# Performance work log

Measured on AMD Instinct MI355X. Metric: run time of the kernel, lower is better.

Reference implementation:

```python
import jax, jax.numpy as jnp
import numpy as np

TEMPERATURE = 0.5


def setup_inputs() -> dict:
    key = jax.random.key(0)
    k1, k2 = jax.random.split(key)
    emb = jax.random.normal(k1, (16384, 128), dtype=jnp.float32)
    emb = emb / jnp.linalg.norm(emb, axis=1, keepdims=True)  # L2-normalized, per docstring
    labels = jax.random.randint(k2, (16384,), 0, 64, dtype=jnp.int64)
    return {"embeddings": emb, "partition_labels": labels}


def reference(embeddings, partition_labels):
    n = embeddings.shape[0]
    # [N, N] similarity matrix, scaled by temperature
    sim = jnp.matmul(embeddings, embeddings.T) / TEMPERATURE
    exp_sim = jnp.exp(sim)
    eye = jnp.eye(n, dtype=bool)
    pos_mask = (partition_labels[None, :] == partition_labels[:, None]) & ~eye
    # numerator: sum of exp over positives; denominator: sum over all k != i
    pos_sum = jnp.sum(jnp.where(pos_mask, exp_sim, 0.0), axis=1)
    all_sum = jnp.sum(jnp.where(~eye, exp_sim, 0.0), axis=1)
    valid = jnp.any(pos_mask, axis=1)
    loss_i = -(jnp.log(pos_sum) - jnp.log(all_sum))
    n_valid = jnp.sum(valid)
    total = jnp.sum(jnp.where(valid, loss_i, 0.0))
    return jnp.where(n_valid > 0, total / n_valid, 0.0)
```

## Files before the change

### kernel.cpp

```cpp
#include <hip/hip_runtime.h>

#define N_EMB 16384
#define DIM 128
#define BM 128
#define BN 128
#define NSPLIT 8
#define CPS (N_EMB / NSPLIT)
#define NCT (CPS / BN)

typedef __bf16 bf16x8 __attribute__((ext_vector_type(8)));
typedef float f32x4 __attribute__((ext_vector_type(4)));
typedef unsigned short us8 __attribute__((ext_vector_type(8)));
typedef unsigned int u32;

#define SCALE 2.8853900817779268f

__device__ inline float fast_exp2(float x) {
#if __has_builtin(__builtin_amdgcn_exp2f)
  return __builtin_amdgcn_exp2f(x);
#else
  return exp2f(x);
#endif
}
__device__ inline float fast_log2(float x) {
#if __has_builtin(__builtin_amdgcn_logf)
  return __builtin_amdgcn_logf(x);
#else
  return log2f(x);
#endif
}

__device__ inline unsigned short f2bf(float f) {
  unsigned int u = __float_as_uint(f);
  u += 0x7fffu + ((u >> 16) & 1u);
  return (unsigned short)(u >> 16);
}

__device__ inline void gll16(const unsigned short* g, unsigned short* l) {
  __builtin_amdgcn_global_load_lds(
      (const __attribute__((address_space(1))) u32*)g,
      (__attribute__((address_space(3))) u32*)l, 16, 0, 0);
}

__device__ inline void stage_tile_fl(const float* __restrict__ src,
                                     unsigned short* __restrict__ dst,
                                     int tid) {
#pragma unroll
  for (int i = 0; i < 8; ++i) {
    int G = i * 256 + tid;
    int col16 = G & 15;
    int quad = (G >> 4) & 3;
    int ks = (G >> 6) & 3;
    int tc = G >> 8;
    const float* p = src + (tc * 16 + col16) * DIM + ks * 32 + quad * 8;
    float4 a = *reinterpret_cast<const float4*>(p);
    float4 b = *reinterpret_cast<const float4*>(p + 4);
    us8 g;
    g[0] = f2bf(a.x); g[1] = f2bf(a.y); g[2] = f2bf(a.z); g[3] = f2bf(a.w);
    g[4] = f2bf(b.x); g[5] = f2bf(b.y); g[6] = f2bf(b.z); g[7] = f2bf(b.w);
    *reinterpret_cast<us8*>(dst + G * 8) = g;
  }
}

__global__ __launch_bounds__(256) void preconv(
    const float* __restrict__ emb, unsigned short* __restrict__ eraw,
    unsigned short* __restrict__ escal) {
  __shared__ unsigned short lds[128 * DIM];
  const int tid = threadIdx.x;
  const size_t base = (size_t)blockIdx.x * (128 * DIM);
  stage_tile_fl(emb + base, lds, tid);
  __syncthreads();
#pragma unroll
  for (int i = 0; i < 8; ++i) {
    int G = i * 256 + tid;
    us8 v = *reinterpret_cast<const us8*>(lds + G * 8);
    *reinterpret_cast<us8*>(eraw + base + G * 8) = v;
    us8 s;
#pragma unroll
    for (int j = 0; j < 8; ++j) {
      float f = __uint_as_float((u32)v[j] << 16) * SCALE;
      s[j] = f2bf(f);
    }
    *reinterpret_cast<us8*>(escal + base + G * 8) = s;
  }
}

__global__ __launch_bounds__(256, 4) void cl_main(
    const unsigned short* __restrict__ eraw,
    const unsigned short* __restrict__ escal,
    const int* __restrict__ labels, float* __restrict__ ws_all,
    float* __restrict__ ws_pos) {
  __shared__ unsigned short lds[BN * DIM];

  const int tid = threadIdx.x;
  const int lane = tid & 63;
  const int w = tid >> 6;
  const int col16 = lane & 15;
  const int quad = lane >> 4;
  const int r0 = blockIdx.x * BM;
  const int cs = blockIdx.y;

  {
    const unsigned short* g = escal + (size_t)r0 * DIM;
#pragma unroll
    for (int i = 0; i < 8; ++i) {
      int chunk = i * 4 + w;
      gll16(g + chunk * 512 + lane * 8, lds + chunk * 512);
    }
  }
  __syncthreads();

  bf16x8 afrag[2][4];
#pragma unroll
  for (int tr = 0; tr < 2; ++tr)
#pragma unroll
    for (int ks = 0; ks < 4; ++ks)
      afrag[tr][ks] = *reinterpret_cast<const bf16x8*>(
          lds + ((w * 2 + tr) * 4 + ks) * 512 + lane * 8);

  int labi[8];
  float all_p[8], pos_p[8];
#pragma unroll
  for (int t = 0; t < 8; ++t) {
    labi[t] = labels[r0 + w * 32 + (t >> 2) * 16 + quad * 4 + (t & 3)];
    all_p[t] = 0.f;
    pos_p[t] = 0.f;
  }

  for (int ct = 0; ct < NCT; ++ct) {
    const int c0 = cs * CPS + ct * BN;
    __syncthreads();
    {
      const unsigned short* g = eraw + (size_t)c0 * DIM;
#pragma unroll
      for (int i = 0; i < 8; ++i) {
        int chunk = i * 4 + w;
        gll16(g + chunk * 512 + lane * 8, lds + chunk * 512);
      }
    }
    __syncthreads();

#pragma unroll
    for (int tc = 0; tc < 8; ++tc) {
      bf16x8 bf[4];
#pragma unroll
      for (int ks = 0; ks < 4; ++ks)
        bf[ks] = *reinterpret_cast<const bf16x8*>(lds + (tc * 4 + ks) * 512 +
                                                  lane * 8);
      int labj = labels[c0 + tc * 16 + col16];
#pragma unroll
      for (int tr = 0; tr < 2; ++tr) {
        f32x4 acc = {0.f, 0.f, 0.f, 0.f};
#pragma unroll
        for (int ks = 0; ks < 4; ++ks)
          acc = __builtin_amdgcn_mfma_f32_16x16x32_bf16(afrag[tr][ks], bf[ks],
                                                        acc, 0, 0, 0);
        const bool diag = (c0 + tc * 16) == (r0 + w * 32 + tr * 16);
#pragma unroll
        for (int r = 0; r < 4; ++r) {
          float e = fast_exp2(acc[r]);
          if (diag && (quad * 4 + r) == col16) e = 0.f;
          all_p[tr * 4 + r] += e;
          pos_p[tr * 4 + r] += (labi[tr * 4 + r] == labj) ? e : 0.f;
        }
      }
    }
  }

#pragma unroll
  for (int t = 0; t < 8; ++t) {
    float a = all_p[t], p = pos_p[t];
#pragma unroll
    for (int m = 8; m >= 1; m >>= 1) {
      a += __shfl_xor(a, m, 64);
      p += __shfl_xor(p, m, 64);
    }
    if (col16 == 0) {
      int row_g = r0 + w * 32 + (t >> 2) * 16 + quad * 4 + (t & 3);
      ws_all[cs * N_EMB + row_g] = a;
      ws_pos[cs * N_EMB + row_g] = p;
    }
  }
}

__global__ __launch_bounds__(1024) void finalize_kernel(
    const float* __restrict__ ws_all, const float* __restrict__ ws_pos,
    float* __restrict__ out) {
  __shared__ float s_t[1024];
  __shared__ int s_c[1024];
  const int tid = threadIdx.x;
  float tot = 0.f;
  int cnt = 0;
  for (int row = tid; row < N_EMB; row += 1024) {
    float a = 0.f, p = 0.f;
#pragma unroll
    for (int s = 0; s < NSPLIT; ++s) {
      a += ws_all[s * N_EMB + row];
      p += ws_pos[s * N_EMB + row];
    }
    if (p > 0.f) {
      tot += fast_log2(a) - fast_log2(p);
      cnt++;
    }
  }
  s_t[tid] = tot;
  s_c[tid] = cnt;
  __syncthreads();
  for (int s = 512; s > 0; s >>= 1) {
    if (tid < s) {
      s_t[tid] += s_t[tid + s];
      s_c[tid] += s_c[tid + s];
    }
    __syncthreads();
  }
  if (tid == 0)
    out[0] =
        (s_c[0] > 0) ? (s_t[0] * 0.6931471805599453f / (float)s_c[0]) : 0.f;
}

extern "C" void kernel_launch(void* const* d_in, const int* in_sizes, int n_in,
                              void* d_out, int out_size, void* d_ws,
                              size_t ws_size, hipStream_t stream) {
  const float* emb = (const float*)d_in[0];
  const int* labels = (const int*)d_in[1];

  unsigned short* eraw = (unsigned short*)d_ws;
  unsigned short* escal = eraw + (size_t)N_EMB * DIM;
  float* ws_all = (float*)(escal + (size_t)N_EMB * DIM);
  float* ws_pos = ws_all + NSPLIT * N_EMB;

  preconv<<<N_EMB / 128, 256, 0, stream>>>(emb, eraw, escal);
  cl_main<<<dim3(N_EMB / BM, NSPLIT), 256, 0, stream>>>(eraw, escal, labels,
                                                        ws_all, ws_pos);
  finalize_kernel<<<1, 1024, 0, stream>>>(ws_all, ws_pos, (float*)d_out);
}
```

Measured before the change: 164.2 us.

## Sort rows by label and compute positive sums only within label groups

Rows are bucketed by label into a permutation, so the dense pass computes only the all-pair exp sums with no label compares or diagonal masking. A separate kernel computes positive sums over the block-diagonal label groups and records the diagonal term, which is subtracted afterwards. The dense kernel also uses 128-thread blocks with each wave holding 64 rows, and the final reduction is split across many blocks. This adds a serial single-block histogram/permutation kernel, extra launches, and a small redundant MFMA pass over the group tiles.

```diff
diff --git a/kernel.cpp b/kernel.cpp
--- a/kernel.cpp
+++ b/kernel.cpp
@@ -2,11 +2,11 @@
 
 #define N_EMB 16384
 #define DIM 128
-#define BM 128
-#define BN 128
 #define NSPLIT 8
 #define CPS (N_EMB / NSPLIT)
+#define BN 128
 #define NCT (CPS / BN)
+#define NLAB 64
 
 typedef __bf16 bf16x8 __attribute__((ext_vector_type(8)));
 typedef float f32x4 __attribute__((ext_vector_type(4)));
@@ -14,6 +14,7 @@
 typedef unsigned int u32;
 
 #define SCALE 2.8853900817779268f
+#define LN2 0.6931471805599453f
 
 __device__ inline float fast_exp2(float x) {
 #if __has_builtin(__builtin_amdgcn_exp2f)
@@ -42,90 +43,89 @@
       (__attribute__((address_space(3))) u32*)l, 16, 0, 0);
 }
 
-__device__ inline void stage_tile_fl(const float* __restrict__ src,
-                                     unsigned short* __restrict__ dst,
-                                     int tid) {
-#pragma unroll
-  for (int i = 0; i < 8; ++i) {
-    int G = i * 256 + tid;
+__global__ __launch_bounds__(1024) void perm_kernel(
+    const int* __restrict__ labels, int* __restrict__ perm,
+    int* __restrict__ gstart) {
+  __shared__ int hist[NLAB];
+  __shared__ int cur[NLAB];
+  const int tid = threadIdx.x;
+  if (tid < NLAB) hist[tid] = 0;
+  __syncthreads();
+  for (int i = tid; i < N_EMB; i += 1024) atomicAdd(&hist[labels[i]], 1);
+  __syncthreads();
+  if (tid == 0) {
+    int s = 0;
+    for (int l = 0; l < NLAB; ++l) {
+      gstart[l] = s;
+      cur[l] = s;
+      s += hist[l];
+    }
+    gstart[NLAB] = s;
+  }
+  __syncthreads();
+  for (int i = tid; i < N_EMB; i += 1024) {
+    int p = atomicAdd(&cur[labels[i]], 1);
+    perm[p] = i;
+  }
+}
+
+__global__ __launch_bounds__(256) void preconv(
+    const float* __restrict__ emb, const int* __restrict__ perm,
+    unsigned short* __restrict__ eraw, unsigned short* __restrict__ escal) {
+  const int tid = threadIdx.x;
+  const int tile = blockIdx.x >> 2;
+  const int part = blockIdx.x & 3;
+  const size_t base = (size_t)tile * (128 * DIM);
+#pragma unroll
+  for (int i = 0; i < 2; ++i) {
+    int G = part * 512 + i * 256 + tid;
     int col16 = G & 15;
-    int quad = (G >> 4) & 3;
+    int qd = (G >> 4) & 3;
     int ks = (G >> 6) & 3;
     int tc = G >> 8;
-    const float* p = src + (tc * 16 + col16) * DIM + ks * 32 + quad * 8;
+    int srow = perm[tile * 128 + tc * 16 + col16];
+    const float* p = emb + (size_t)srow * DIM + ks * 32 + qd * 8;
     float4 a = *reinterpret_cast<const float4*>(p);
     float4 b = *reinterpret_cast<const float4*>(p + 4);
-    us8 g;
+    us8 g, s;
     g[0] = f2bf(a.x); g[1] = f2bf(a.y); g[2] = f2bf(a.z); g[3] = f2bf(a.w);
     g[4] = f2bf(b.x); g[5] = f2bf(b.y); g[6] = f2bf(b.z); g[7] = f2bf(b.w);
-    *reinterpret_cast<us8*>(dst + G * 8) = g;
-  }
-}
-
-__global__ __launch_bounds__(256) void preconv(
-    const float* __restrict__ emb, unsigned short* __restrict__ eraw,
-    unsigned short* __restrict__ escal) {
-  __shared__ unsigned short lds[128 * DIM];
-  const int tid = threadIdx.x;
-  const size_t base = (size_t)blockIdx.x * (128 * DIM);
-  stage_tile_fl(emb + base, lds, tid);
-  __syncthreads();
-#pragma unroll
-  for (int i = 0; i < 8; ++i) {
-    int G = i * 256 + tid;
-    us8 v = *reinterpret_cast<const us8*>(lds + G * 8);
-    *reinterpret_cast<us8*>(eraw + base + G * 8) = v;
-    us8 s;
 #pragma unroll
     for (int j = 0; j < 8; ++j) {
-      float f = __uint_as_float((u32)v[j] << 16) * SCALE;
+      float f = __uint_as_float((u32)g[j] << 16) * SCALE;
       s[j] = f2bf(f);
     }
-    *reinterpret_cast<us8*>(escal + base + G * 8) = s;
-  }
-}
-
-__global__ __launch_bounds__(256, 4) void cl_main(
+    *reinterpret_cast<us8*>(eraw + base + (size_t)G * 8) = g;
+    *reinterpret_cast<us8*>(escal + base + (size_t)G * 8) = s;
+  }
+}
+
+__global__ __launch_bounds__(128, 2) void cl_all(
     const unsigned short* __restrict__ eraw,
-    const unsigned short* __restrict__ escal,
-    const int* __restrict__ labels, float* __restrict__ ws_all,
-    float* __restrict__ ws_pos) {
+    const unsigned short* __restrict__ escal, float* __restrict__ ws_all) {
   __shared__ unsigned short lds[BN * DIM];
-
   const int tid = threadIdx.x;
   const int lane = tid & 63;
   const int w = tid >> 6;
   const int col16 = lane & 15;
   const int quad = lane >> 4;
-  const int r0 = blockIdx.x * BM;
+  const int r0 = blockIdx.x * 128;
   const int cs = blockIdx.y;
 
-  {
-    const unsigned short* g = escal + (size_t)r0 * DIM;
-#pragma unroll
-    for (int i = 0; i < 8; ++i) {
-      int chunk = i * 4 + w;
-      gll16(g + chunk * 512 + lane * 8, lds + chunk * 512);
-    }
-  }
-  __syncthreads();
-
-  bf16x8 afrag[2][4];
-#pragma unroll
-  for (int tr = 0; tr < 2; ++tr)
+  bf16x8 afrag[4][4];
+#pragma unroll
+  for (int tr = 0; tr < 4; ++tr) {
+    const int T = (r0 >> 4) + w * 4 + tr;
+    const unsigned short* p = escal + (size_t)(T >> 3) * (128 * DIM) +
+                              ((T & 7) * 4) * 512 + lane * 8;
 #pragma unroll
     for (int ks = 0; ks < 4; ++ks)
-      afrag[tr][ks] = *reinterpret_cast<const bf16x8*>(
-          lds + ((w * 2 + tr) * 4 + ks) * 512 + lane * 8);
-
-  int labi[8];
-  float all_p[8], pos_p[8];
-#pragma unroll
-  for (int t = 0; t < 8; ++t) {
-    labi[t] = labels[r0 + w * 32 + (t >> 2) * 16 + quad * 4 + (t & 3)];
-    all_p[t] = 0.f;
-    pos_p[t] = 0.f;
-  }
+      afrag[tr][ks] = *reinterpret_cast<const bf16x8*>(p + ks * 512);
+  }
+
+  float all_p[16];
+#pragma unroll
+  for (int t = 0; t < 16; ++t) all_p[t] = 0.f;
 
   for (int ct = 0; ct < NCT; ++ct) {
     const int c0 = cs * CPS + ct * BN;
@@ -133,8 +133,8 @@
     {
       const unsigned short* g = eraw + (size_t)c0 * DIM;
 #pragma unroll
-      for (int i = 0; i < 8; ++i) {
-        int chunk = i * 4 + w;
+      for (int i = 0; i < 16; ++i) {
+        int chunk = i * 2 + w;
         gll16(g + chunk * 512 + lane * 8, lds + chunk * 512);
       }
     }
@@ -142,80 +142,146 @@
 
 #pragma unroll
     for (int tc = 0; tc < 8; ++tc) {
-      bf16x8 bf[4];
+      bf16x8 bfr[4];
 #pragma unroll
       for (int ks = 0; ks < 4; ++ks)
-        bf[ks] = *reinterpret_cast<const bf16x8*>(lds + (tc * 4 + ks) * 512 +
-                                                  lane * 8);
-      int labj = labels[c0 + tc * 16 + col16];
-#pragma unroll
-      for (int tr = 0; tr < 2; ++tr) {
+        bfr[ks] = *reinterpret_cast<const bf16x8*>(lds + (tc * 4 + ks) * 512 +
+                                                   lane * 8);
+#pragma unroll
+      for (int tr = 0; tr < 4; ++tr) {
         f32x4 acc = {0.f, 0.f, 0.f, 0.f};
 #pragma unroll
         for (int ks = 0; ks < 4; ++ks)
-          acc = __builtin_amdgcn_mfma_f32_16x16x32_bf16(afrag[tr][ks], bf[ks],
+          acc = __builtin_amdgcn_mfma_f32_16x16x32_bf16(afrag[tr][ks], bfr[ks],
                                                         acc, 0, 0, 0);
-        const bool diag = (c0 + tc * 16) == (r0 + w * 32 + tr * 16);
-#pragma unroll
-        for (int r = 0; r < 4; ++r) {
-          float e = fast_exp2(acc[r]);
-          if (diag && (quad * 4 + r) == col16) e = 0.f;
-          all_p[tr * 4 + r] += e;
-          pos_p[tr * 4 + r] += (labi[tr * 4 + r] == labj) ? e : 0.f;
+#pragma unroll
+        for (int r = 0; r < 4; ++r)
+          all_p[tr * 4 + r] += fast_exp2(acc[r]);
+      }
+    }
+  }
+
+#pragma unroll
+  for (int t = 0; t < 16; ++t) {
+    float a = all_p[t];
+#pragma unroll
+    for (int m = 8; m >= 1; m >>= 1) a += __shfl_xor(a, m, 64);
+    if (col16 == 0) {
+      int row_g = r0 + w * 64 + (t >> 2) * 16 + quad * 4 + (t & 3);
+      ws_all[cs * N_EMB + row_g] = a;
+    }
+  }
+}
+
+__global__ __launch_bounds__(256) void cl_pos(
+    const unsigned short* __restrict__ eraw,
+    const unsigned short* __restrict__ escal, const int* __restrict__ gstart,
+    float* __restrict__ ws_pos, float* __restrict__ ws_diag) {
+  const int l = blockIdx.x;
+  const int chunk = blockIdx.y;
+  const int gs = gstart[l], ge = gstart[l + 1];
+  const int tid = threadIdx.x;
+  const int lane = tid & 63;
+  const int w = tid >> 6;
+  const int col16 = lane & 15;
+  const int quad = lane >> 4;
+  const int t0 = gs >> 4;
+  const int t1 = (ge + 15) >> 4;
+
+  for (int ta = t0 + chunk * 4 + w; ta < t1; ta += 16) {
+    bf16x8 af[4];
+    const unsigned short* pa = escal + (size_t)(ta >> 3) * (128 * DIM) +
+                               ((ta & 7) * 4) * 512 + lane * 8;
+#pragma unroll
+    for (int ks = 0; ks < 4; ++ks)
+      af[ks] = *reinterpret_cast<const bf16x8*>(pa + ks * 512);
+    const int grow = ta * 16 + quad * 4;
+    float posr[4] = {0.f, 0.f, 0.f, 0.f};
+
+    for (int tb = t0; tb < t1; ++tb) {
+      bf16x8 bfr[4];
+      const unsigned short* pb = eraw + (size_t)(tb >> 3) * (128 * DIM) +
+                                 ((tb & 7) * 4) * 512 + lane * 8;
+#pragma unroll
+      for (int ks = 0; ks < 4; ++ks)
+        bfr[ks] = *reinterpret_cast<const bf16x8*>(pb + ks * 512);
+      f32x4 acc = {0.f, 0.f, 0.f, 0.f};
+#pragma unroll
+      for (int ks = 0; ks < 4; ++ks)
+        acc = __builtin_amdgcn_mfma_f32_16x16x32_bf16(af[ks], bfr[ks], acc, 0,
+                                                      0, 0);
+      const int gcol = tb * 16 + col16;
+      const bool colin = (gcol >= gs) && (gcol < ge);
+#pragma unroll
+      for (int r = 0; r < 4; ++r) {
+        float e = fast_exp2(acc[r]);
+        const int gr = grow + r;
+        if (gcol == gr) {
+          if (colin) ws_diag[gr] = e;
+        } else if (colin) {
+          posr[r] += e;
         }
       }
     }
-  }
-
-#pragma unroll
-  for (int t = 0; t < 8; ++t) {
-    float a = all_p[t], p = pos_p[t];
-#pragma unroll
-    for (int m = 8; m >= 1; m >>= 1) {
-      a += __shfl_xor(a, m, 64);
-      p += __shfl_xor(p, m, 64);
-    }
-    if (col16 == 0) {
-      int row_g = r0 + w * 32 + (t >> 2) * 16 + quad * 4 + (t & 3);
-      ws_all[cs * N_EMB + row_g] = a;
-      ws_pos[cs * N_EMB + row_g] = p;
-    }
-  }
-}
-
-__global__ __launch_bounds__(1024) void finalize_kernel(
+
+#pragma unroll
+    for (int r = 0; r < 4; ++r) {
+      float p = posr[r];
+#pragma unroll
+      for (int m = 8; m >= 1; m >>= 1) p += __shfl_xor(p, m, 64);
+      const int gr = grow + r;
+      if (col16 == 0 && gr >= gs && gr < ge) ws_pos[gr] = p;
+    }
+  }
+}
+
+__global__ __launch_bounds__(256) void fin1(
     const float* __restrict__ ws_all, const float* __restrict__ ws_pos,
-    float* __restrict__ out) {
-  __shared__ float s_t[1024];
-  __shared__ int s_c[1024];
-  const int tid = threadIdx.x;
-  float tot = 0.f;
-  int cnt = 0;
-  for (int row = tid; row < N_EMB; row += 1024) {
-    float a = 0.f, p = 0.f;
-#pragma unroll
-    for (int s = 0; s < NSPLIT; ++s) {
-      a += ws_all[s * N_EMB + row];
-      p += ws_pos[s * N_EMB + row];
-    }
-    if (p > 0.f) {
-      tot += fast_log2(a) - fast_log2(p);
-      cnt++;
-    }
-  }
-  s_t[tid] = tot;
-  s_c[tid] = cnt;
+    const float* __restrict__ ws_diag, float* __restrict__ part_tot,
+    int* __restrict__ part_cnt) {
+  __shared__ float s_t[256];
+  __shared__ int s_c[256];
+  const int tid = threadIdx.x;
+  const int row = blockIdx.x * 256 + tid;
+  float a = 0.f;
+#pragma unroll
+  for (int s = 0; s < NSPLIT; ++s) a += ws_all[s * N_EMB + row];
+  a -= ws_diag[row];
+  const float p = ws_pos[row];
+  float t = 0.f;
+  int c = 0;
+  if (p > 0.f) {
+    t = fast_log2(a) - fast_log2(p);
+    c = 1;
+  }
+  s_t[tid] = t;
+  s_c[tid] = c;
   __syncthreads();
-  for (int s = 512; s > 0; s >>= 1) {
+  for (int s = 128; s > 0; s >>= 1) {
     if (tid < s) {
       s_t[tid] += s_t[tid + s];
       s_c[tid] += s_c[tid + s];
     }
     __syncthreads();
   }
-  if (tid == 0)
-    out[0] =
-        (s_c[0] > 0) ? (s_t[0] * 0.6931471805599453f / (float)s_c[0]) : 0.f;
+  if (tid == 0) {
+    part_tot[blockIdx.x] = s_t[0];
+    part_cnt[blockIdx.x] = s_c[0];
+  }
+}
+
+__global__ __launch_bounds__(64) void fin2(const float* __restrict__ part_tot,
+                                           const int* __restrict__ part_cnt,
+                                           float* __restrict__ out) {
+  const int tid = threadIdx.x;
+  float t = part_tot[tid];
+  int c = part_cnt[tid];
+#pragma unroll
+  for (int m = 32; m >= 1; m >>= 1) {
+    t += __shfl_xor(t, m, 64);
+    c += __shfl_xor(c, m, 64);
+  }
+  if (tid == 0) out[0] = (c > 0) ? (t * LN2 / (float)c) : 0.f;
 }
 
 extern "C" void kernel_launch(void* const* d_in, const int* in_sizes, int n_in,
@@ -228,9 +294,18 @@
   unsigned short* escal = eraw + (size_t)N_EMB * DIM;
   float* ws_all = (float*)(escal + (size_t)N_EMB * DIM);
   float* ws_pos = ws_all + NSPLIT * N_EMB;
-
-  preconv<<<N_EMB / 128, 256, 0, stream>>>(emb, eraw, escal);
-  cl_main<<<dim3(N_EMB / BM, NSPLIT), 256, 0, stream>>>(eraw, escal, labels,
-                                                        ws_all, ws_pos);
-  finalize_kernel<<<1, 1024, 0, stream>>>(ws_all, ws_pos, (float*)d_out);
-}
+  float* ws_diag = ws_pos + N_EMB;
+  float* part_tot = ws_diag + N_EMB;
+  int* part_cnt = (int*)(part_tot + 64);
+  int* perm = part_cnt + 64;
+  int* gstart = perm + N_EMB;
+
+  perm_kernel<<<1, 1024, 0, stream>>>(labels, perm, gstart);
+  preconv<<<512, 256, 0, stream>>>(emb, perm, eraw, escal);
+  cl_all<<<dim3(N_EMB / 128, NSPLIT), 128, 0, stream>>>(eraw, escal, ws_all);
+  cl_pos<<<dim3(NLAB, 4), 256, 0, stream>>>(eraw, escal, gstart, ws_pos,
+                                            ws_diag);
+  fin1<<<N_EMB / 256, 256, 0, stream>>>(ws_all, ws_pos, ws_diag, part_tot,
+                                        part_cnt);
+  fin2<<<1, 64, 0, stream>>>(part_tot, part_cnt, (float*)d_out);
+}
```

Result: slower. 169.0 us (+2.9%).

## Use 2-wave blocks with 64 rows per wave and scale A fragments in-register

Applied to the files above, without the earlier changes.

The main kernel now runs 128-thread blocks in which each wave owns 64 rows (4 row tiles), so each B fragment read from LDS feeds twice as many MFMAs. The A fragments are loaded straight from global memory and scaled in registers, which removes the separate scaled copy from preconv. Preconv is split over four times as many blocks and writes directly without an LDS round trip. The workspace is transposed to row-major per split so finalize can use float4 loads. The cost is twice the register footprint per wave and half as many waves per block, which may reduce latency hiding for the B-tile loads and the exp work.

```diff
diff --git a/kernel.cpp b/kernel.cpp
--- a/kernel.cpp
+++ b/kernel.cpp
@@ -2,10 +2,9 @@
 
 #define N_EMB 16384
 #define DIM 128
-#define BM 128
-#define BN 128
 #define NSPLIT 8
 #define CPS (N_EMB / NSPLIT)
+#define BN 128
 #define NCT (CPS / BN)
 
 typedef __bf16 bf16x8 __attribute__((ext_vector_type(8)));
@@ -14,6 +13,7 @@
 typedef unsigned int u32;
 
 #define SCALE 2.8853900817779268f
+#define LN2 0.6931471805599453f
 
 __device__ inline float fast_exp2(float x) {
 #if __has_builtin(__builtin_amdgcn_exp2f)
@@ -42,87 +42,66 @@
       (__attribute__((address_space(3))) u32*)l, 16, 0, 0);
 }
 
-__device__ inline void stage_tile_fl(const float* __restrict__ src,
-                                     unsigned short* __restrict__ dst,
-                                     int tid) {
-#pragma unroll
-  for (int i = 0; i < 8; ++i) {
-    int G = i * 256 + tid;
+__global__ __launch_bounds__(256) void preconv(
+    const float* __restrict__ emb, unsigned short* __restrict__ eraw) {
+  const int tid = threadIdx.x;
+  const int tile = blockIdx.x >> 2;
+  const int part = blockIdx.x & 3;
+  const size_t base = (size_t)tile * (128 * DIM);
+#pragma unroll
+  for (int i = 0; i < 2; ++i) {
+    int G = part * 512 + i * 256 + tid;
     int col16 = G & 15;
-    int quad = (G >> 4) & 3;
+    int qd = (G >> 4) & 3;
     int ks = (G >> 6) & 3;
     int tc = G >> 8;
-    const float* p = src + (tc * 16 + col16) * DIM + ks * 32 + quad * 8;
+    int srow = tile * 128 + tc * 16 + col16;
+    const float* p = emb + (size_t)srow * DIM + ks * 32 + qd * 8;
     float4 a = *reinterpret_cast<const float4*>(p);
     float4 b = *reinterpret_cast<const float4*>(p + 4);
     us8 g;
     g[0] = f2bf(a.x); g[1] = f2bf(a.y); g[2] = f2bf(a.z); g[3] = f2bf(a.w);
     g[4] = f2bf(b.x); g[5] = f2bf(b.y); g[6] = f2bf(b.z); g[7] = f2bf(b.w);
-    *reinterpret_cast<us8*>(dst + G * 8) = g;
-  }
-}
-
-__global__ __launch_bounds__(256) void preconv(
-    const float* __restrict__ emb, unsigned short* __restrict__ eraw,
-    unsigned short* __restrict__ escal) {
-  __shared__ unsigned short lds[128 * DIM];
-  const int tid = threadIdx.x;
-  const size_t base = (size_t)blockIdx.x * (128 * DIM);
-  stage_tile_fl(emb + base, lds, tid);
-  __syncthreads();
-#pragma unroll
-  for (int i = 0; i < 8; ++i) {
-    int G = i * 256 + tid;
-    us8 v = *reinterpret_cast<const us8*>(lds + G * 8);
-    *reinterpret_cast<us8*>(eraw + base + G * 8) = v;
-    us8 s;
-#pragma unroll
-    for (int j = 0; j < 8; ++j) {
-      float f = __uint_as_float((u32)v[j] << 16) * SCALE;
-      s[j] = f2bf(f);
-    }
-    *reinterpret_cast<us8*>(escal + base + G * 8) = s;
-  }
-}
-
-__global__ __launch_bounds__(256, 4) void cl_main(
-    const unsigned short* __restrict__ eraw,
-    const unsigned short* __restrict__ escal,
-    const int* __restrict__ labels, float* __restrict__ ws_all,
-    float* __restrict__ ws_pos) {
+    *reinterpret_cast<us8*>(eraw + base + (size_t)G * 8) = g;
+  }
+}
+
+__device__ inline bf16x8 load_scaled(const unsigned short* p) {
+  us8 v = *reinterpret_cast<const us8*>(p);
+  us8 s;
+#pragma unroll
+  for (int j = 0; j < 8; ++j)
+    s[j] = f2bf(__uint_as_float((u32)v[j] << 16) * SCALE);
+  return *reinterpret_cast<bf16x8*>(&s);
+}
+
+__global__ __launch_bounds__(128) void cl_main(
+    const unsigned short* __restrict__ eraw, const int* __restrict__ labels,
+    float* __restrict__ ws_all, float* __restrict__ ws_pos) {
   __shared__ unsigned short lds[BN * DIM];
-
   const int tid = threadIdx.x;
   const int lane = tid & 63;
   const int w = tid >> 6;
   const int col16 = lane & 15;
   const int quad = lane >> 4;
-  const int r0 = blockIdx.x * BM;
+  const int r0 = blockIdx.x * 128;
   const int cs = blockIdx.y;
 
-  {
-    const unsigned short* g = escal + (size_t)r0 * DIM;
-#pragma unroll
-    for (int i = 0; i < 8; ++i) {
-      int chunk = i * 4 + w;
-      gll16(g + chunk * 512 + lane * 8, lds + chunk * 512);
-    }
-  }
-  __syncthreads();
-
-  bf16x8 afrag[2][4];
-#pragma unroll
-  for (int tr = 0; tr < 2; ++tr)
-#pragma unroll
-    for (int ks = 0; ks < 4; ++ks)
-      afrag[tr][ks] = *reinterpret_cast<const bf16x8*>(
-          lds + ((w * 2 + tr) * 4 + ks) * 512 + lane * 8);
-
-  int labi[8];
-  float all_p[8], pos_p[8];
-#pragma unroll
-  for (int t = 0; t < 8; ++t) {
-    labi[t] = labels[r0 + w * 32 + (t >> 2) * 16 + quad * 4 + (t & 3)];
+  bf16x8 afrag[4][4];
+#pragma unroll
+  for (int tr = 0; tr < 4; ++tr) {
+    const int T = (r0 >> 4) + w * 4 + tr;
+    const unsigned short* p = eraw + (size_t)(T >> 3) * (128 * DIM) +
+                              ((T & 7) * 4) * 512 + lane * 8;
+#pragma unroll
+    for (int ks = 0; ks < 4; ++ks) afrag[tr][ks] = load_scaled(p + ks * 512);
+  }
+
+  int labi[16];
+  float all_p[16], pos_p[16];
+#pragma unroll
+  for (int t = 0; t < 16; ++t) {
+    labi[t] = labels[r0 + w * 64 + (t >> 2) * 16 + quad * 4 + (t & 3)];
     all_p[t] = 0.f;
     pos_p[t] = 0.f;
   }
@@ -131,10 +110,10 @@
     const int c0 = cs * CPS + ct * BN;
     __syncthreads();
     {
-      const unsigned short* g = eraw + (size_t)c0 * DIM;
-#pragma unroll
-      for (int i = 0; i < 8; ++i) {
-        int chunk = i * 4 + w;
+      const unsigned short* g = eraw + (size_t)(c0 >> 7) * (128 * DIM);
+#pragma unroll
+      for (int i = 0; i < 16; ++i) {
+        int chunk = i * 2 + w;
         gll16(g + chunk * 512 + lane * 8, lds + chunk * 512);
       }
     }
@@ -142,20 +121,20 @@
 
 #pragma unroll
     for (int tc = 0; tc < 8; ++tc) {
-      bf16x8 bf[4];
+      bf16x8 bfr[4];
 #pragma unroll
       for (int ks = 0; ks < 4; ++ks)
-        bf[ks] = *reinterpret_cast<const bf16x8*>(lds + (tc * 4 + ks) * 512 +
-                                                  lane * 8);
-      int labj = labels[c0 + tc * 16 + col16];
-#pragma unroll
-      for (int tr = 0; tr < 2; ++tr) {
+        bfr[ks] = *reinterpret_cast<const bf16x8*>(lds + (tc * 4 + ks) * 512 +
+                                                   lane * 8);
+      const int labj = labels[c0 + tc * 16 + col16];
+#pragma unroll
+      for (int tr = 0; tr < 4; ++tr) {
         f32x4 acc = {0.f, 0.f, 0.f, 0.f};
 #pragma unroll
         for (int ks = 0; ks < 4; ++ks)
-          acc = __builtin_amdgcn_mfma_f32_16x16x32_bf16(afrag[tr][ks], bf[ks],
+          acc = __builtin_amdgcn_mfma_f32_16x16x32_bf16(afrag[tr][ks], bfr[ks],
                                                         acc, 0, 0, 0);
-        const bool diag = (c0 + tc * 16) == (r0 + w * 32 + tr * 16);
+        const bool diag = (c0 + tc * 16) == (r0 + w * 64 + tr * 16);
 #pragma unroll
         for (int r = 0; r < 4; ++r) {
           float e = fast_exp2(acc[r]);
@@ -168,7 +147,7 @@
   }
 
 #pragma unroll
-  for (int t = 0; t < 8; ++t) {
+  for (int t = 0; t < 16; ++t) {
     float a = all_p[t], p = pos_p[t];
 #pragma unroll
     for (int m = 8; m >= 1; m >>= 1) {
@@ -176,27 +155,31 @@
       p += __shfl_xor(p, m, 64);
     }
     if (col16 == 0) {
-      int row_g = r0 + w * 32 + (t >> 2) * 16 + quad * 4 + (t & 3);
-      ws_all[cs * N_EMB + row_g] = a;
-      ws_pos[cs * N_EMB + row_g] = p;
-    }
-  }
-}
-
-__global__ __launch_bounds__(1024) void finalize_kernel(
-    const float* __restrict__ ws_all, const float* __restrict__ ws_pos,
-    float* __restrict__ out) {
+      int row_g = r0 + w * 64 + (t >> 2) * 16 + quad * 4 + (t & 3);
+      ws_all[(size_t)row_g * NSPLIT + cs] = a;
+      ws_pos[(size_t)row_g * NSPLIT + cs] = p;
+    }
+  }
+}
+
+__global__ __launch_bounds__(1024) void fin(const float* __restrict__ ws_all,
+                                            const float* __restrict__ ws_pos,
+                                            float* __restrict__ out) {
   __shared__ float s_t[1024];
   __shared__ int s_c[1024];
   const int tid = threadIdx.x;
   float tot = 0.f;
   int cnt = 0;
   for (int row = tid; row < N_EMB; row += 1024) {
+    const float4* pa = reinterpret_cast<const float4*>(ws_all + (size_t)row * NSPLIT);
+    const float4* pp = reinterpret_cast<const float4*>(ws_pos + (size_t)row * NSPLIT);
     float a = 0.f, p = 0.f;
 #pragma unroll
-    for (int s = 0; s < NSPLIT; ++s) {
-      a += ws_all[s * N_EMB + row];
-      p += ws_pos[s * N_EMB + row];
+    for (int q = 0; q < NSPLIT / 4; ++q) {
+      float4 va = pa[q];
+      float4 vp = pp[q];
+      a += va.x + va.y + va.z + va.w;
+      p += vp.x + vp.y + vp.z + vp.w;
     }
     if (p > 0.f) {
       tot += fast_log2(a) - fast_log2(p);
@@ -214,8 +197,7 @@
     __syncthreads();
   }
   if (tid == 0)
-    out[0] =
-        (s_c[0] > 0) ? (s_t[0] * 0.6931471805599453f / (float)s_c[0]) : 0.f;
+    out[0] = (s_c[0] > 0) ? (s_t[0] * LN2 / (float)s_c[0]) : 0.f;
 }
 
 extern "C" void kernel_launch(void* const* d_in, const int* in_sizes, int n_in,
@@ -225,12 +207,10 @@
   const int* labels = (const int*)d_in[1];
 
   unsigned short* eraw = (unsigned short*)d_ws;
-  unsigned short* escal = eraw + (size_t)N_EMB * DIM;
-  float* ws_all = (float*)(escal + (size_t)N_EMB * DIM);
-  float* ws_pos = ws_all + NSPLIT * N_EMB;
-
-  preconv<<<N_EMB / 128, 256, 0, stream>>>(emb, eraw, escal);
-  cl_main<<<dim3(N_EMB / BM, NSPLIT), 256, 0, stream>>>(eraw, escal, labels,
-                                                        ws_all, ws_pos);
-  finalize_kernel<<<1, 1024, 0, stream>>>(ws_all, ws_pos, (float*)d_out);
-}
+  float* ws_all = (float*)(eraw + (size_t)N_EMB * DIM);
+  float* ws_pos = ws_all + (size_t)N_EMB * NSPLIT;
+
+  preconv<<<512, 256, 0, stream>>>(emb, eraw);
+  cl_main<<<dim3(128, NSPLIT), 128, 0, stream>>>(eraw, labels, ws_all, ws_pos);
+  fin<<<1, 1024, 0, stream>>>(ws_all, ws_pos, (float*)d_out);
+}
```

Result: slower. 173.8 us (+5.9%).
